# Kernel optimization log

Measured on AMD Instinct MI355X. Metric: run time of the kernel, lower is better.

## Reference

```python
import jax, jax.numpy as jnp
import numpy as np


def _greens(x, k0_raw, amp_raw):
    """Faithful TunableGreens: FFT-domain filtering with per-channel-pair Green's fn.
    NOTE: the source applies fftn over axes (0,1) (batch+H) but ifftn over axes (1,2)
    (H+W); we replicate that exactly."""
    H, W = x.shape[1], x.shape[2]
    k0 = jax.nn.softplus(k0_raw)    # (C, Co, 1, 1)
    amp = jax.nn.softplus(amp_raw)  # (C, Co, 1, 1)
    fy = (2.0 * jnp.pi) * jnp.fft.fftfreq(H, d=1.0).astype(jnp.float32)
    fx = (2.0 * jnp.pi) * jnp.fft.fftfreq(W, d=1.0).astype(jnp.float32)
    p = fy[:, None] ** 2 + fx[None, :] ** 2            # (H, W) = sum(freq_grid**2, -1)
    g_fourier = 1.0 / (amp * p - k0 - 1j)              # (C, Co, H, W) complex64
    u_fft = jnp.fft.fftn(x, axes=(0, 1))               # axes (0,1) as in source
    u_filtered = jnp.einsum('bijc,coij->bijo', u_fft, g_fourier)
    return jnp.fft.ifftn(u_filtered, axes=(1, 2)).real


def _D(Wm, x):
    # per-pixel channel mixing: x [b,i,j,c], Wm [b,i,j,c,o]
    return jnp.einsum('bijc,bijco->bijo', x, Wm)


def _project(k, W1, b1, W2, b2, W3, b3):
    act = lambda z: jnp.exp(-z ** 2)
    x = act(k @ W1 + b1)
    x = act(x @ W2 + b2)
    return x @ W3 + b3


def setup_inputs() -> dict:
    key = jax.random.key(0)
    ks = jax.random.split(key, 10)
    B, H, W, C = 2, 128, 128, 32
    d = {}
    d['u'] = jax.random.normal(ks[0], (B, H, W, C), jnp.float32)
    d['k'] = jax.random.normal(ks[1], (B, H, W, 1), jnp.float32)
    for i, n in enumerate(['g1', 'g2', 'g3', 'g4']):
        d[n] = jax.random.normal(ks[2 + i], (B, H, W, C, C), jnp.float32) * 0.1
    # Project MLP params (lecun-normal-ish scaling)
    d['W1'] = jax.random.normal(ks[6], (1, C), jnp.float32)
    d['b1'] = jnp.zeros((C,), jnp.float32)
    d['W2'] = jax.random.normal(ks[7], (C, C), jnp.float32) * (1.0 / np.sqrt(C))
    d['b2'] = jnp.zeros((C,), jnp.float32)
    d['W3'] = jax.random.normal(ks[8], (C, C), jnp.float32) * (1.0 / np.sqrt(C))
    d['b3'] = jnp.zeros((C,), jnp.float32)
    # TunableGreens params, constant(1.0) init as in source
    d['k0_G'] = jnp.ones((C, C, 1, 1), jnp.float32)
    d['amp_G'] = jnp.ones((C, C, 1, 1), jnp.float32)
    d['k0_Gs'] = jnp.ones((C, C, 1, 1), jnp.float32)
    d['amp_Gs'] = jnp.ones((C, C, 1, 1), jnp.float32)
    return d


def reference(u, k, g1, g2, g3, g4, W1, b1, W2, b2, W3, b3,
              k0_G, amp_G, k0_Gs, amp_Gs):
    s = _project(k, W1, b1, W2, b2, W3, b3)           # [B,H,W,C]
    u1 = _D(g4, _greens(s, k0_Gs, amp_Gs))
    u2 = _D(g1, _greens(_D(g2, u), k0_G, amp_G)) + _D(g3, u)
    return u1 + u2
```

## Files before the change

kernel.cpp:

```cpp
#include <hip/hip_runtime.h>

using u16 = unsigned short;
using u32 = unsigned int;

#define PI2 6.283185307179586f

struct cpx { float x, y; };

__device__ __forceinline__ float bf2f(u16 h){ return __uint_as_float(((u32)h) << 16); }
__device__ __forceinline__ u16 f2bf(float f){
  u32 u = __float_as_uint(f);
  u = u + 0x7fffu + ((u >> 16) & 1u);
  return (u16)(u >> 16);
}

__device__ __forceinline__ float ldv(const void* base, size_t i, int md){
  return md ? ((const float*)base)[i] : bf2f(((const u16*)base)[i]);
}

__device__ __forceinline__ cpx cadd(cpx a, cpx b){ return {a.x+b.x, a.y+b.y}; }
__device__ __forceinline__ cpx csub(cpx a, cpx b){ return {a.x-b.x, a.y-b.y}; }
__device__ __forceinline__ cpx cmul(cpx a, cpx b){ return {a.x*b.x - a.y*b.y, a.x*b.y + a.y*b.x}; }
__device__ __forceinline__ int br6(int l){ return (int)(__brev((u32)l) >> 26); }
__device__ __forceinline__ cpx shflx(cpx v, int m){
  cpx r; r.x = __shfl_xor(v.x, m, 64); r.y = __shfl_xor(v.y, m, 64); return r;
}

__device__ __forceinline__ void make_tw(int l, cpx tw[6]){
  #pragma unroll
  for (int s = 0; s < 6; s++){
    int h = 64 >> s;
    float ang = -PI2 * (float)(l & (h-1)) / (float)(2*h);
    float sv, cv; sincosf(ang, &sv, &cv);
    tw[s] = {cv, sv};
  }
}

__device__ __forceinline__ void fft_fwd(cpx& v0, cpx& v1, int l, const cpx tw[6]){
  cpx a = cadd(v0, v1), b = csub(v0, v1);
  v0 = a; v1 = cmul(b, tw[0]);
  #pragma unroll
  for (int s = 1; s < 6; s++){
    int h = 64 >> s;
    cpx p0 = shflx(v0, h), p1 = shflx(v1, h);
    bool up = (l & h) != 0;
    cpx n0 = up ? cmul(csub(p0, v0), tw[s]) : cadd(v0, p0);
    cpx n1 = up ? cmul(csub(p1, v1), tw[s]) : cadd(v1, p1);
    v0 = n0; v1 = n1;
  }
  { cpx p0 = shflx(v0, 1), p1 = shflx(v1, 1);
    bool up = (l & 1) != 0;
    v0 = up ? csub(p0, v0) : cadd(v0, p0);
    v1 = up ? csub(p1, v1) : cadd(v1, p1); }
}

__device__ __forceinline__ void fft_inv(cpx& v0, cpx& v1, int l, const cpx tw[6]){
  { cpx p0 = shflx(v0, 1), p1 = shflx(v1, 1);
    bool up = (l & 1) != 0;
    v0 = up ? csub(p0, v0) : cadd(v0, p0);
    v1 = up ? csub(p1, v1) : cadd(v1, p1); }
  #pragma unroll
  for (int s = 5; s >= 1; s--){
    int h = 64 >> s;
    cpx twc = {tw[s].x, -tw[s].y};
    cpx p0 = shflx(v0, h), p1 = shflx(v1, h);
    bool up = (l & h) != 0;
    cpx t0 = cmul(up ? v0 : p0, twc);
    cpx t1 = cmul(up ? v1 : p1, twc);
    v0 = up ? csub(p0, t0) : cadd(v0, t0);
    v1 = up ? csub(p1, t1) : cadd(v1, t1);
  }
  { cpx twc = {tw[0].x, -tw[0].y};
    cpx t = cmul(v1, twc);
    cpx n0 = cadd(v0, t), n1 = csub(v0, t);
    v0 = n0; v1 = n1; }
}

__device__ __forceinline__ float softplusf(float x){ return (x > 20.0f) ? x : log1pf(expf(x)); }

__device__ __forceinline__ void acc8_bf(uint4 a, uint4 b, float x0, float x1, float acc[8]){
  acc[0] = fmaf(x0, __uint_as_float(a.x << 16),         acc[0]);
  acc[1] = fmaf(x0, __uint_as_float(a.x & 0xffff0000u), acc[1]);
  acc[2] = fmaf(x0, __uint_as_float(a.y << 16),         acc[2]);
  acc[3] = fmaf(x0, __uint_as_float(a.y & 0xffff0000u), acc[3]);
  acc[4] = fmaf(x0, __uint_as_float(a.z << 16),         acc[4]);
  acc[5] = fmaf(x0, __uint_as_float(a.z & 0xffff0000u), acc[5]);
  acc[6] = fmaf(x0, __uint_as_float(a.w << 16),         acc[6]);
  acc[7] = fmaf(x0, __uint_as_float(a.w & 0xffff0000u), acc[7]);
  acc[0] = fmaf(x1, __uint_as_float(b.x << 16),         acc[0]);
  acc[1] = fmaf(x1, __uint_as_float(b.x & 0xffff0000u), acc[1]);
  acc[2] = fmaf(x1, __uint_as_float(b.y << 16),         acc[2]);
  acc[3] = fmaf(x1, __uint_as_float(b.y & 0xffff0000u), acc[3]);
  acc[4] = fmaf(x1, __uint_as_float(b.z << 16),         acc[4]);
  acc[5] = fmaf(x1, __uint_as_float(b.z & 0xffff0000u), acc[5]);
  acc[6] = fmaf(x1, __uint_as_float(b.w << 16),         acc[6]);
  acc[7] = fmaf(x1, __uint_as_float(b.w & 0xffff0000u), acc[7]);
}
__device__ __forceinline__ void acc8_f32(float4 a0, float4 a1, float4 b0, float4 b1,
                                         float x0, float x1, float acc[8]){
  acc[0] = fmaf(x0, a0.x, acc[0]); acc[1] = fmaf(x0, a0.y, acc[1]);
  acc[2] = fmaf(x0, a0.z, acc[2]); acc[3] = fmaf(x0, a0.w, acc[3]);
  acc[4] = fmaf(x0, a1.x, acc[4]); acc[5] = fmaf(x0, a1.y, acc[5]);
  acc[6] = fmaf(x0, a1.z, acc[6]); acc[7] = fmaf(x0, a1.w, acc[7]);
  acc[0] = fmaf(x1, b0.x, acc[0]); acc[1] = fmaf(x1, b0.y, acc[1]);
  acc[2] = fmaf(x1, b0.z, acc[2]); acc[3] = fmaf(x1, b0.w, acc[3]);
  acc[4] = fmaf(x1, b1.x, acc[4]); acc[5] = fmaf(x1, b1.y, acc[5]);
  acc[6] = fmaf(x1, b1.z, acc[6]); acc[7] = fmaf(x1, b1.w, acc[7]);
}

__global__ void k_detect(const void* g1, int* flag){
  __shared__ int cnt;
  if (threadIdx.x == 0) cnt = 0;
  __syncthreads();
  const u16* p = (const u16*)g1;
  int local = 0;
  for (int i = threadIdx.x; i < 4096; i += 256){
    float v = bf2f(p[i]);
    if (!(fabsf(v) < 100.0f)) local++;
  }
  atomicAdd(&cnt, local);
  __syncthreads();
  if (threadIdx.x == 0) *flag = (cnt > 64) ? 1 : 0;
}

__global__ void k_tabs(const void* k0G, const void* ampG, const void* k0Gs, const void* ampGs,
                       float* tabs, const int* flag){
  int md = *flag;
  for (int i = threadIdx.x; i < 1024; i += 256){
    tabs[i]        = softplusf(ldv(ampGs, i, md));
    tabs[1024 + i] = softplusf(ldv(k0Gs, i, md));
    tabs[2048 + i] = softplusf(ldv(ampG, i, md));
    tabs[3072 + i] = softplusf(ldv(k0G, i, md));
  }
}

__global__ __launch_bounds__(256) void k_project(const void* kin, const void* W1, const void* b1,
    const void* W2, const void* b2, const void* W3, const void* b3, float* S, const int* flag){
  __shared__ float sW2[1024], sW3[1024], sml[128];
  int md = *flag;
  int t = threadIdx.x;
  for (int i = t; i < 1024; i += 256){ sW2[i] = ldv(W2, i, md); sW3[i] = ldv(W3, i, md); }
  if (t < 32){
    sml[t]     = ldv(W1, t, md); sml[32+t] = ldv(b1, t, md);
    sml[64+t]  = ldv(b2, t, md); sml[96+t] = ldv(b3, t, md);
  }
  __syncthreads();
  int pix = blockIdx.x * 256 + t;
  float kv = ldv(kin, pix, md);
  float a1[32], a2[32];
  #pragma unroll
  for (int c = 0; c < 32; c++){ float z = fmaf(kv, sml[c], sml[32+c]); a1[c] = expf(-z*z); }
  for (int o = 0; o < 32; o++){
    float z = sml[64+o];
    #pragma unroll
    for (int c = 0; c < 32; c++) z = fmaf(a1[c], sW2[c*32+o], z);
    a2[o] = expf(-z*z);
  }
  for (int o = 0; o < 32; o++){
    float sv = sml[96+o];
    #pragma unroll
    for (int c = 0; c < 32; c++) sv = fmaf(a2[c], sW3[c*32+o], sv);
    S[(size_t)pix*32 + o] = sv;
  }
}

__global__ __launch_bounds__(256) void k_dmat(const void* u, const void* g2, float* D, const int* flag){
  int md = *flag;
  int t = threadIdx.x, l = t & 63;
  size_t pix = (size_t)blockIdx.x * 8 + (size_t)(t >> 6) * 2;
  int c32 = l & 31, ch = l >> 2;
  float xa = ldv(u, pix*32 + c32, md);
  float xb = ldv(u, (pix+1)*32 + c32, md);
  float acc0[8] = {0.f,0.f,0.f,0.f,0.f,0.f,0.f,0.f};
  float acc1[8] = {0.f,0.f,0.f,0.f,0.f,0.f,0.f,0.f};
  if (md){
    const float4* Ra = (const float4*)((const float*)g2 + pix*1024);
    const float4* Rb = (const float4*)((const float*)g2 + (pix+1)*1024);
    float4 aa = Ra[2*l], ab = Ra[2*l+1], ac = Ra[128+2*l], ad = Ra[128+2*l+1];
    float4 ba = Rb[2*l], bb = Rb[2*l+1], bc = Rb[128+2*l], bd = Rb[128+2*l+1];
    float xa0 = __shfl(xa, ch, 64), xa1 = __shfl(xa, 16+ch, 64);
    float xb0 = __shfl(xb, ch, 64), xb1 = __shfl(xb, 16+ch, 64);
    acc8_f32(aa, ab, ac, ad, xa0, xa1, acc0);
    acc8_f32(ba, bb, bc, bd, xb0, xb1, acc1);
  } else {
    const uint4* Ra = (const uint4*)((const u16*)g2 + pix*1024);
    const uint4* Rb = (const uint4*)((const u16*)g2 + (pix+1)*1024);
    uint4 a0 = Ra[l], a1 = Ra[64+l];
    uint4 b0 = Rb[l], b1 = Rb[64+l];
    float xa0 = __shfl(xa, ch, 64), xa1 = __shfl(xa, 16+ch, 64);
    float xb0 = __shfl(xb, ch, 64), xb1 = __shfl(xb, 16+ch, 64);
    acc8_bf(a0, a1, xa0, xa1, acc0);
    acc8_bf(b0, b1, xb0, xb1, acc1);
  }
  #pragma unroll
  for (int d = 4; d <= 32; d <<= 1){
    #pragma unroll
    for (int jj = 0; jj < 8; jj++){
      acc0[jj] += __shfl_xor(acc0[jj], d, 64);
      acc1[jj] += __shfl_xor(acc1[jj], d, 64);
    }
  }
  if (l < 4){
    ((float4*)(D + pix*32))[2*l]       = make_float4(acc0[0], acc0[1], acc0[2], acc0[3]);
    ((float4*)(D + pix*32))[2*l+1]     = make_float4(acc0[4], acc0[5], acc0[6], acc0[7]);
    ((float4*)(D + (pix+1)*32))[2*l]   = make_float4(acc1[0], acc1[1], acc1[2], acc1[3]);
    ((float4*)(D + (pix+1)*32))[2*l+1] = make_float4(acc1[4], acc1[5], acc1[6], acc1[7]);
  }
}

__global__ __launch_bounds__(512) void kg_a(const float* S, const float* Dd, const float* tabs, float2* Q){
  __shared__ __align__(16) cpx E[64*128];
  int t = threadIdx.x;
  int p = blockIdx.x >> 7, j = blockIdx.x & 127;
  const float* X = p ? Dd : S;
  const float* ampT = tabs + p*2048;
  const float* k0T  = ampT + 1024;
  int l = t & 63, w = t >> 6;
  cpx tw[6]; make_tw(l, tw);

  {
    int h = t >> 2, ch = (t & 3) * 8;
    const float4* x0 = (const float4*)(X + (((size_t)h)*128 + j)*32 + ch);
    const float4* x1 = (const float4*)(X + (((size_t)(128 + h))*128 + j)*32 + ch);
    #pragma unroll
    for (int q = 0; q < 2; q++){
      float4 A = x0[q], B = x1[q];
      int c = ch + q*4;
      E[(c+0)*128 + h] = {A.x+B.x, 0.f};  E[(32+c+0)*128 + h] = {A.x-B.x, 0.f};
      E[(c+1)*128 + h] = {A.y+B.y, 0.f};  E[(32+c+1)*128 + h] = {A.y-B.y, 0.f};
      E[(c+2)*128 + h] = {A.z+B.z, 0.f};  E[(32+c+2)*128 + h] = {A.z-B.z, 0.f};
      E[(c+3)*128 + h] = {A.w+B.w, 0.f};  E[(32+c+3)*128 + h] = {A.w-B.w, 0.f};
    }
  }
  __syncthreads();
  for (int c = w; c < 64; c += 8){
    cpx* col = E + c*128;
    cpx v0 = col[l], v1 = col[l+64];
    fft_fwd(v0, v1, l, tw);
    ((float4*)col)[br6(l)] = make_float4(v0.x, v0.y, v1.x, v1.y);
  }
  __syncthreads();
  {
    int o = t & 31, ig = t >> 5;
    float aT[32], kT[32];
    #pragma unroll
    for (int c = 0; c < 32; c++){ aT[c] = ampT[c*32+o]; kT[c] = k0T[c*32+o]; }
    float fj = (j < 64) ? (float)j : (float)(j - 128);
    fj *= (PI2 / 128.0f);
    float px = fj * fj;
    for (int chunk = 0; chunk < 2; chunk++){
      cpx y0[4], y1[4];
      #pragma unroll
      for (int q = 0; q < 4; q++){
        int i = ig + 16*(chunk*4 + q);
        float fi = (i < 64) ? (float)i : (float)(i - 128);
        fi *= (PI2 / 128.0f);
        float pp = fmaf(fi, fi, px);
        cpx a0 = {0.f, 0.f}, a1 = {0.f, 0.f};
        #pragma unroll
        for (int c = 0; c < 32; c++){
          float dd  = fmaf(aT[c], pp, -kT[c]);
          float inv = __builtin_amdgcn_rcpf(fmaf(dd, dd, 1.0f));
          float gr = dd * inv, gi = inv;
          cpx x0 = E[c*128 + i];
          cpx x1 = E[(32+c)*128 + i];
          a0.x = fmaf(x0.x, gr, fmaf(-x0.y, gi, a0.x));
          a0.y = fmaf(x0.x, gi, fmaf( x0.y, gr, a0.y));
          a1.x = fmaf(x1.x, gr, fmaf(-x1.y, gi, a1.x));
          a1.y = fmaf(x1.x, gi, fmaf( x1.y, gr, a1.y));
        }
        y0[q] = a0; y1[q] = a1;
      }
      __syncthreads();
      #pragma unroll
      for (int q = 0; q < 4; q++){
        int i = ig + 16*(chunk*4 + q);
        E[o*128 + i]      = y0[q];
        E[(32+o)*128 + i] = y1[q];
      }
      __syncthreads();
    }
  }
  for (int cidx = w; cidx < 64; cidx += 8){
    cpx* col = E + cidx*128;
    float4 tv = ((const float4*)col)[br6(l)];
    cpx v0 = {tv.x, tv.y}, v1 = {tv.z, tv.w};
    fft_inv(v0, v1, l, tw);
    const float sc = 1.0f/128.0f;
    col[l]    = {v0.x*sc, v0.y*sc};
    col[l+64] = {v1.x*sc, v1.y*sc};
  }
  __syncthreads();
  {
    int o = t & 31, bb = (t >> 5) & 1, yb = t >> 6;
    for (int m = 0; m < 16; m++){
      int y = yb + 8*m;
      cpx v = E[(bb*32+o)*128 + y];
      Q[((((size_t)(p*2+bb))*128 + y)*128 + j)*32 + o] = make_float2(v.x, v.y);
    }
  }
}

__global__ __launch_bounds__(256) void kg_c(const float2* Q, float* G0, float* G1){
  __shared__ __align__(16) cpx Z[32*128];
  __shared__ float R[32*128];
  int t = threadIdx.x, l = t & 63, w = t >> 6;
  int idx = blockIdx.x;
  int p = idx >> 8, rem = idx & 255, bb = rem >> 7, y = rem & 127;
  cpx tw[6]; make_tw(l, tw);
  const float4* src = (const float4*)(Q + ((size_t)((p*2+bb)*128 + y))*4096);
  for (int q = t; q < 2048; q += 256){
    float4 v = src[q];
    int m = q*2, jj = m >> 5, c = m & 31;
    Z[c*128 + jj]     = {v.x, v.y};
    Z[(c+1)*128 + jj] = {v.z, v.w};
  }
  __syncthreads();
  for (int c = w; c < 32; c += 4){
    cpx* col = Z + c*128;
    float4 tv = ((const float4*)col)[br6(l)];
    cpx v0 = {tv.x, tv.y}, v1 = {tv.z, tv.w};
    fft_inv(v0, v1, l, tw);
    R[c*128 + l]      = v0.x * (1.0f/128.0f);
    R[c*128 + l + 64] = v1.x * (1.0f/128.0f);
  }
  __syncthreads();
  float* dst = (p ? G1 : G0) + ((size_t)(bb*128 + y))*4096;
  int jj = t >> 3, c4 = (t & 7)*4;
  for (int rep = 0; rep < 4; rep++){
    int j2 = jj + rep*32;
    float4 o4 = { R[(c4+0)*128 + j2], R[(c4+1)*128 + j2],
                  R[(c4+2)*128 + j2], R[(c4+3)*128 + j2] };
    ((float4*)(dst + (size_t)j2*32))[c4 >> 2] = o4;
  }
}

__global__ __launch_bounds__(256) void k_final(const void* u, const void* g1, const void* g3, const void* g4,
    const float* G0, const float* G1, void* out, const int* flag){
  int md = *flag;
  int t = threadIdx.x, l = t & 63;
  size_t pix = (size_t)blockIdx.x * 4 + (t >> 6);
  int c32 = l & 31, ch = l >> 2;
  float xs = G0[pix*32 + c32];
  float xm = G1[pix*32 + c32];
  float xu = ldv(u, pix*32 + c32, md);
  float acc[8] = {0.f,0.f,0.f,0.f,0.f,0.f,0.f,0.f};
  if (md){
    const float4* R4 = (const float4*)((const float*)g4 + pix*1024);
    const float4* R1 = (const float4*)((const float*)g1 + pix*1024);
    const float4* R3 = (const float4*)((const float*)g3 + pix*1024);
    float4 p4a = R4[2*l], p4b = R4[2*l+1], q4a = R4[128+2*l], q4b = R4[128+2*l+1];
    float4 p1a = R1[2*l], p1b = R1[2*l+1], q1a = R1[128+2*l], q1b = R1[128+2*l+1];
    float4 p3a = R3[2*l], p3b = R3[2*l+1], q3a = R3[128+2*l], q3b = R3[128+2*l+1];
    float xs0 = __shfl(xs, ch, 64), xs1 = __shfl(xs, 16+ch, 64);
    float xm0 = __shfl(xm, ch, 64), xm1 = __shfl(xm, 16+ch, 64);
    float xu0 = __shfl(xu, ch, 64), xu1 = __shfl(xu, 16+ch, 64);
    acc8_f32(p4a, p4b, q4a, q4b, xs0, xs1, acc);
    acc8_f32(p1a, p1b, q1a, q1b, xm0, xm1, acc);
    acc8_f32(p3a, p3b, q3a, q3b, xu0, xu1, acc);
  } else {
    const uint4* R4 = (const uint4*)((const u16*)g4 + pix*1024);
    const uint4* R1 = (const uint4*)((const u16*)g1 + pix*1024);
    const uint4* R3 = (const uint4*)((const u16*)g3 + pix*1024);
    uint4 a4 = R4[l], b4 = R4[64+l];
    uint4 a1 = R1[l], b1 = R1[64+l];
    uint4 a3 = R3[l], b3 = R3[64+l];
    float xs0 = __shfl(xs, ch, 64), xs1 = __shfl(xs, 16+ch, 64);
    float xm0 = __shfl(xm, ch, 64), xm1 = __shfl(xm, 16+ch, 64);
    float xu0 = __shfl(xu, ch, 64), xu1 = __shfl(xu, 16+ch, 64);
    acc8_bf(a4, b4, xs0, xs1, acc);
    acc8_bf(a1, b1, xm0, xm1, acc);
    acc8_bf(a3, b3, xu0, xu1, acc);
  }
  #pragma unroll
  for (int d = 4; d <= 32; d <<= 1){
    #pragma unroll
    for (int jj = 0; jj < 8; jj++) acc[jj] += __shfl_xor(acc[jj], d, 64);
  }
  if (l < 4){
    if (md){
      float4 o0 = {acc[0], acc[1], acc[2], acc[3]};
      float4 o1 = {acc[4], acc[5], acc[6], acc[7]};
      ((float4*)out)[pix*8 + 2*l]     = o0;
      ((float4*)out)[pix*8 + 2*l + 1] = o1;
    } else {
      uint4 v;
      v.x = (u32)f2bf(acc[0]) | ((u32)f2bf(acc[1]) << 16);
      v.y = (u32)f2bf(acc[2]) | ((u32)f2bf(acc[3]) << 16);
      v.z = (u32)f2bf(acc[4]) | ((u32)f2bf(acc[5]) << 16);
      v.w = (u32)f2bf(acc[6]) | ((u32)f2bf(acc[7]) << 16);
      ((uint4*)out)[pix*4 + l] = v;
    }
  }
}

extern "C" void kernel_launch(void* const* d_in, const int* in_sizes, int n_in,
                              void* d_out, int out_size, void* d_ws, size_t ws_size,
                              hipStream_t stream){
  (void)in_sizes; (void)n_in; (void)out_size; (void)ws_size;
  const void* u    = d_in[0];
  const void* kk   = d_in[1];
  const void* g1   = d_in[2];
  const void* g2   = d_in[3];
  const void* g3   = d_in[4];
  const void* g4   = d_in[5];
  const void* W1   = d_in[6];
  const void* b1   = d_in[7];
  const void* W2   = d_in[8];
  const void* b2   = d_in[9];
  const void* W3   = d_in[10];
  const void* b3   = d_in[11];
  const void* k0G  = d_in[12];
  const void* ampG = d_in[13];
  const void* k0Gs = d_in[14];
  const void* ampGs= d_in[15];

  float* ws   = (float*)d_ws;
  float* S    = ws;
  float* Dd   = ws + (1u<<20);
  float2* Q   = (float2*)(ws + 2*(1u<<20));
  float* G0   = ws + 6*(1u<<20);
  float* G1b  = ws + 7*(1u<<20);
  float* tabs = ws + 8*(1u<<20);
  int*   flag = (int*)(tabs + 4096);

  k_detect <<<1,    256, 0, stream>>>(g1, flag);
  k_tabs   <<<1,    256, 0, stream>>>(k0G, ampG, k0Gs, ampGs, tabs, flag);
  k_project<<<128,  256, 0, stream>>>(kk, W1, b1, W2, b2, W3, b3, S, flag);
  k_dmat   <<<4096, 256, 0, stream>>>(u, g2, Dd, flag);
  kg_a     <<<256,  512, 0, stream>>>(S, Dd, tabs, Q);
  kg_c     <<<512,  256, 0, stream>>>(Q, G0, G1b);
  k_final  <<<8192, 256, 0, stream>>>(u, g1, g3, g4, G0, G1b, (void*)d_out, flag);
}
```

Measured before the change: 536.7 us.

## Software-pipeline per-pixel mixing kernels over multiple pixels per wave and pad FFT LDS

k_dmat and k_final now have each wave process several consecutive pixels (8 and 4), prefetching the next pixel's weight rows and inputs into registers while computing the current one, with grid sizes reduced to match. This targets memory latency in the bandwidth-bound channel-mixing kernels. kg_c pads its shared-memory column strides to cut LDS bank conflicts in the transpose and output gather. The prefetching raises register pressure, which may lower occupancy.

After: 541.5 us. About the same (+0.9%).

```diff
diff --git a/kernel.cpp b/kernel.cpp
--- a/kernel.cpp
+++ b/kernel.cpp
@@ -167,44 +167,85 @@
 __global__ __launch_bounds__(256) void k_dmat(const void* u, const void* g2, float* D, const int* flag){
   int md = *flag;
   int t = threadIdx.x, l = t & 63;
-  size_t pix = (size_t)blockIdx.x * 8 + (size_t)(t >> 6) * 2;
+  int wid = blockIdx.x * 4 + (t >> 6);
+  size_t base = (size_t)wid * 8;
   int c32 = l & 31, ch = l >> 2;
-  float xa = ldv(u, pix*32 + c32, md);
-  float xb = ldv(u, (pix+1)*32 + c32, md);
-  float acc0[8] = {0.f,0.f,0.f,0.f,0.f,0.f,0.f,0.f};
-  float acc1[8] = {0.f,0.f,0.f,0.f,0.f,0.f,0.f,0.f};
-  if (md){
-    const float4* Ra = (const float4*)((const float*)g2 + pix*1024);
-    const float4* Rb = (const float4*)((const float*)g2 + (pix+1)*1024);
-    float4 aa = Ra[2*l], ab = Ra[2*l+1], ac = Ra[128+2*l], ad = Ra[128+2*l+1];
-    float4 ba = Rb[2*l], bb = Rb[2*l+1], bc = Rb[128+2*l], bd = Rb[128+2*l+1];
-    float xa0 = __shfl(xa, ch, 64), xa1 = __shfl(xa, 16+ch, 64);
-    float xb0 = __shfl(xb, ch, 64), xb1 = __shfl(xb, 16+ch, 64);
-    acc8_f32(aa, ab, ac, ad, xa0, xa1, acc0);
-    acc8_f32(ba, bb, bc, bd, xb0, xb1, acc1);
+  const u16* U16 = (const u16*)u;
+  const float* U32 = (const float*)u;
+  if (!md){
+    const uint4* R = (const uint4*)((const u16*)g2 + base*1024);
+    uint4 a0 = R[l], a1 = R[64+l], b0 = R[128+l], b1 = R[192+l];
+    float xa = bf2f(U16[base*32 + c32]);
+    float xb = bf2f(U16[(base+1)*32 + c32]);
+    #pragma unroll
+    for (int it = 0; it < 4; it++){
+      int nit = (it < 3) ? it + 1 : it;
+      uint4 na0 = R[nit*256 + l],       na1 = R[nit*256 + 64 + l];
+      uint4 nb0 = R[nit*256 + 128 + l], nb1 = R[nit*256 + 192 + l];
+      float nxa = bf2f(U16[(base + 2*nit)*32 + c32]);
+      float nxb = bf2f(U16[(base + 2*nit + 1)*32 + c32]);
+      float xa0 = __shfl(xa, ch, 64), xa1 = __shfl(xa, 16+ch, 64);
+      float xb0 = __shfl(xb, ch, 64), xb1 = __shfl(xb, 16+ch, 64);
+      float acc0[8] = {0.f,0.f,0.f,0.f,0.f,0.f,0.f,0.f};
+      float acc1[8] = {0.f,0.f,0.f,0.f,0.f,0.f,0.f,0.f};
+      acc8_bf(a0, a1, xa0, xa1, acc0);
+      acc8_bf(b0, b1, xb0, xb1, acc1);
+      #pragma unroll
+      for (int d = 4; d <= 32; d <<= 1){
+        #pragma unroll
+        for (int jj = 0; jj < 8; jj++){
+          acc0[jj] += __shfl_xor(acc0[jj], d, 64);
+          acc1[jj] += __shfl_xor(acc1[jj], d, 64);
+        }
+      }
+      size_t p0 = base + 2*it, p1 = p0 + 1;
+      if (l < 4){
+        ((float4*)(D + p0*32))[2*l]   = make_float4(acc0[0], acc0[1], acc0[2], acc0[3]);
+        ((float4*)(D + p0*32))[2*l+1] = make_float4(acc0[4], acc0[5], acc0[6], acc0[7]);
+        ((float4*)(D + p1*32))[2*l]   = make_float4(acc1[0], acc1[1], acc1[2], acc1[3]);
+        ((float4*)(D + p1*32))[2*l+1] = make_float4(acc1[4], acc1[5], acc1[6], acc1[7]);
+      }
+      a0 = na0; a1 = na1; b0 = nb0; b1 = nb1; xa = nxa; xb = nxb;
+    }
   } else {
-    const uint4* Ra = (const uint4*)((const u16*)g2 + pix*1024);
-    const uint4* Rb = (const uint4*)((const u16*)g2 + (pix+1)*1024);
-    uint4 a0 = Ra[l], a1 = Ra[64+l];
-    uint4 b0 = Rb[l], b1 = Rb[64+l];
-    float xa0 = __shfl(xa, ch, 64), xa1 = __shfl(xa, 16+ch, 64);
-    float xb0 = __shfl(xb, ch, 64), xb1 = __shfl(xb, 16+ch, 64);
-    acc8_bf(a0, a1, xa0, xa1, acc0);
-    acc8_bf(b0, b1, xb0, xb1, acc1);
-  }
-  #pragma unroll
-  for (int d = 4; d <= 32; d <<= 1){
-    #pragma unroll
-    for (int jj = 0; jj < 8; jj++){
-      acc0[jj] += __shfl_xor(acc0[jj], d, 64);
-      acc1[jj] += __shfl_xor(acc1[jj], d, 64);
-    }
-  }
-  if (l < 4){
-    ((float4*)(D + pix*32))[2*l]       = make_float4(acc0[0], acc0[1], acc0[2], acc0[3]);
-    ((float4*)(D + pix*32))[2*l+1]     = make_float4(acc0[4], acc0[5], acc0[6], acc0[7]);
-    ((float4*)(D + (pix+1)*32))[2*l]   = make_float4(acc1[0], acc1[1], acc1[2], acc1[3]);
-    ((float4*)(D + (pix+1)*32))[2*l+1] = make_float4(acc1[4], acc1[5], acc1[6], acc1[7]);
+    const float4* R = (const float4*)((const float*)g2 + base*1024);
+    float4 a0 = R[2*l], a1 = R[2*l+1], a2 = R[128+2*l], a3 = R[128+2*l+1];
+    float4 b0 = R[256+2*l], b1 = R[256+2*l+1], b2 = R[384+2*l], b3 = R[384+2*l+1];
+    float xa = U32[base*32 + c32];
+    float xb = U32[(base+1)*32 + c32];
+    #pragma unroll
+    for (int it = 0; it < 4; it++){
+      int nit = (it < 3) ? it + 1 : it;
+      const float4* Rn = R + nit*512;
+      float4 na0 = Rn[2*l], na1 = Rn[2*l+1], na2 = Rn[128+2*l], na3 = Rn[128+2*l+1];
+      float4 nb0 = Rn[256+2*l], nb1 = Rn[256+2*l+1], nb2 = Rn[384+2*l], nb3 = Rn[384+2*l+1];
+      float nxa = U32[(base + 2*nit)*32 + c32];
+      float nxb = U32[(base + 2*nit + 1)*32 + c32];
+      float xa0 = __shfl(xa, ch, 64), xa1 = __shfl(xa, 16+ch, 64);
+      float xb0 = __shfl(xb, ch, 64), xb1 = __shfl(xb, 16+ch, 64);
+      float acc0[8] = {0.f,0.f,0.f,0.f,0.f,0.f,0.f,0.f};
+      float acc1[8] = {0.f,0.f,0.f,0.f,0.f,0.f,0.f,0.f};
+      acc8_f32(a0, a1, a2, a3, xa0, xa1, acc0);
+      acc8_f32(b0, b1, b2, b3, xb0, xb1, acc1);
+      #pragma unroll
+      for (int d = 4; d <= 32; d <<= 1){
+        #pragma unroll
+        for (int jj = 0; jj < 8; jj++){
+          acc0[jj] += __shfl_xor(acc0[jj], d, 64);
+          acc1[jj] += __shfl_xor(acc1[jj], d, 64);
+        }
+      }
+      size_t p0 = base + 2*it, p1 = p0 + 1;
+      if (l < 4){
+        ((float4*)(D + p0*32))[2*l]   = make_float4(acc0[0], acc0[1], acc0[2], acc0[3]);
+        ((float4*)(D + p0*32))[2*l+1] = make_float4(acc0[4], acc0[5], acc0[6], acc0[7]);
+        ((float4*)(D + p1*32))[2*l]   = make_float4(acc1[0], acc1[1], acc1[2], acc1[3]);
+        ((float4*)(D + p1*32))[2*l+1] = make_float4(acc1[4], acc1[5], acc1[6], acc1[7]);
+      }
+      a0 = na0; a1 = na1; a2 = na2; a3 = na3;
+      b0 = nb0; b1 = nb1; b2 = nb2; b3 = nb3;
+      xa = nxa; xb = nxb;
+    }
   }
 }
 
@@ -301,9 +342,11 @@
   }
 }
 
+#define ZS 130
+#define RS 133
 __global__ __launch_bounds__(256) void kg_c(const float2* Q, float* G0, float* G1){
-  __shared__ __align__(16) cpx Z[32*128];
-  __shared__ float R[32*128];
+  __shared__ __align__(16) cpx Z[32*ZS];
+  __shared__ float R[32*RS];
   int t = threadIdx.x, l = t & 63, w = t >> 6;
   int idx = blockIdx.x;
   int p = idx >> 8, rem = idx & 255, bb = rem >> 7, y = rem & 127;
@@ -312,25 +355,25 @@
   for (int q = t; q < 2048; q += 256){
     float4 v = src[q];
     int m = q*2, jj = m >> 5, c = m & 31;
-    Z[c*128 + jj]     = {v.x, v.y};
-    Z[(c+1)*128 + jj] = {v.z, v.w};
+    Z[c*ZS + jj]     = {v.x, v.y};
+    Z[(c+1)*ZS + jj] = {v.z, v.w};
   }
   __syncthreads();
   for (int c = w; c < 32; c += 4){
-    cpx* col = Z + c*128;
+    cpx* col = Z + c*ZS;
     float4 tv = ((const float4*)col)[br6(l)];
     cpx v0 = {tv.x, tv.y}, v1 = {tv.z, tv.w};
     fft_inv(v0, v1, l, tw);
-    R[c*128 + l]      = v0.x * (1.0f/128.0f);
-    R[c*128 + l + 64] = v1.x * (1.0f/128.0f);
+    R[c*RS + l]      = v0.x * (1.0f/128.0f);
+    R[c*RS + l + 64] = v1.x * (1.0f/128.0f);
   }
   __syncthreads();
   float* dst = (p ? G1 : G0) + ((size_t)(bb*128 + y))*4096;
   int jj = t >> 3, c4 = (t & 7)*4;
   for (int rep = 0; rep < 4; rep++){
     int j2 = jj + rep*32;
-    float4 o4 = { R[(c4+0)*128 + j2], R[(c4+1)*128 + j2],
-                  R[(c4+2)*128 + j2], R[(c4+3)*128 + j2] };
+    float4 o4 = { R[(c4+0)*RS + j2], R[(c4+1)*RS + j2],
+                  R[(c4+2)*RS + j2], R[(c4+3)*RS + j2] };
     ((float4*)(dst + (size_t)j2*32))[c4 >> 2] = o4;
   }
 }
@@ -339,57 +382,95 @@
     const float* G0, const float* G1, void* out, const int* flag){
   int md = *flag;
   int t = threadIdx.x, l = t & 63;
-  size_t pix = (size_t)blockIdx.x * 4 + (t >> 6);
+  int wid = blockIdx.x * 4 + (t >> 6);
+  size_t base = (size_t)wid * 4;
   int c32 = l & 31, ch = l >> 2;
-  float xs = G0[pix*32 + c32];
-  float xm = G1[pix*32 + c32];
-  float xu = ldv(u, pix*32 + c32, md);
-  float acc[8] = {0.f,0.f,0.f,0.f,0.f,0.f,0.f,0.f};
-  if (md){
-    const float4* R4 = (const float4*)((const float*)g4 + pix*1024);
-    const float4* R1 = (const float4*)((const float*)g1 + pix*1024);
-    const float4* R3 = (const float4*)((const float*)g3 + pix*1024);
+  if (!md){
+    const u16* U = (const u16*)u;
+    const uint4* R4 = (const uint4*)((const u16*)g4 + base*1024);
+    const uint4* R1 = (const uint4*)((const u16*)g1 + base*1024);
+    const uint4* R3 = (const uint4*)((const u16*)g3 + base*1024);
+    uint4 a4 = R4[l], b4 = R4[64+l];
+    uint4 a1 = R1[l], b1 = R1[64+l];
+    uint4 a3 = R3[l], b3 = R3[64+l];
+    float xs = G0[base*32 + c32], xm = G1[base*32 + c32], xu = bf2f(U[base*32 + c32]);
+    #pragma unroll
+    for (int it = 0; it < 4; it++){
+      int nit = (it < 3) ? it + 1 : it;
+      uint4 na4 = R4[nit*128 + l], nb4 = R4[nit*128 + 64 + l];
+      uint4 na1 = R1[nit*128 + l], nb1 = R1[nit*128 + 64 + l];
+      uint4 na3 = R3[nit*128 + l], nb3 = R3[nit*128 + 64 + l];
+      float nxs = G0[(base+nit)*32 + c32];
+      float nxm = G1[(base+nit)*32 + c32];
+      float nxu = bf2f(U[(base+nit)*32 + c32]);
+      float xs0 = __shfl(xs, ch, 64), xs1 = __shfl(xs, 16+ch, 64);
+      float xm0 = __shfl(xm, ch, 64), xm1 = __shfl(xm, 16+ch, 64);
+      float xu0 = __shfl(xu, ch, 64), xu1 = __shfl(xu, 16+ch, 64);
+      float acc[8] = {0.f,0.f,0.f,0.f,0.f,0.f,0.f,0.f};
+      acc8_bf(a4, b4, xs0, xs1, acc);
+      acc8_bf(a1, b1, xm0, xm1, acc);
+      acc8_bf(a3, b3, xu0, xu1, acc);
+      #pragma unroll
+      for (int d = 4; d <= 32; d <<= 1){
+        #pragma unroll
+        for (int jj = 0; jj < 8; jj++) acc[jj] += __shfl_xor(acc[jj], d, 64);
+      }
+      size_t pix = base + it;
+      if (l < 4){
+        uint4 v;
+        v.x = (u32)f2bf(acc[0]) | ((u32)f2bf(acc[1]) << 16);
+        v.y = (u32)f2bf(acc[2]) | ((u32)f2bf(acc[3]) << 16);
+        v.z = (u32)f2bf(acc[4]) | ((u32)f2bf(acc[5]) << 16);
+        v.w = (u32)f2bf(acc[6]) | ((u32)f2bf(acc[7]) << 16);
+        ((uint4*)out)[pix*4 + l] = v;
+      }
+      a4 = na4; b4 = nb4; a1 = na1; b1 = nb1; a3 = na3; b3 = nb3;
+      xs = nxs; xm = nxm; xu = nxu;
+    }
+  } else {
+    const float* U = (const float*)u;
+    const float4* R4 = (const float4*)((const float*)g4 + base*1024);
+    const float4* R1 = (const float4*)((const float*)g1 + base*1024);
+    const float4* R3 = (const float4*)((const float*)g3 + base*1024);
     float4 p4a = R4[2*l], p4b = R4[2*l+1], q4a = R4[128+2*l], q4b = R4[128+2*l+1];
     float4 p1a = R1[2*l], p1b = R1[2*l+1], q1a = R1[128+2*l], q1b = R1[128+2*l+1];
     float4 p3a = R3[2*l], p3b = R3[2*l+1], q3a = R3[128+2*l], q3b = R3[128+2*l+1];
-    float xs0 = __shfl(xs, ch, 64), xs1 = __shfl(xs, 16+ch, 64);
-    float xm0 = __shfl(xm, ch, 64), xm1 = __shfl(xm, 16+ch, 64);
-    float xu0 = __shfl(xu, ch, 64), xu1 = __shfl(xu, 16+ch, 64);
-    acc8_f32(p4a, p4b, q4a, q4b, xs0, xs1, acc);
-    acc8_f32(p1a, p1b, q1a, q1b, xm0, xm1, acc);
-    acc8_f32(p3a, p3b, q3a, q3b, xu0, xu1, acc);
-  } else {
-    const uint4* R4 = (const uint4*)((const u16*)g4 + pix*1024);
-    const uint4* R1 = (const uint4*)((const u16*)g1 + pix*1024);
-    const uint4* R3 = (const uint4*)((const u16*)g3 + pix*1024);
-    uint4 a4 = R4[l], b4 = R4[64+l];
-    uint4 a1 = R1[l], b1 = R1[64+l];
-    uint4 a3 = R3[l], b3 = R3[64+l];
-    float xs0 = __shfl(xs, ch, 64), xs1 = __shfl(xs, 16+ch, 64);
-    float xm0 = __shfl(xm, ch, 64), xm1 = __shfl(xm, 16+ch, 64);
-    float xu0 = __shfl(xu, ch, 64), xu1 = __shfl(xu, 16+ch, 64);
-    acc8_bf(a4, b4, xs0, xs1, acc);
-    acc8_bf(a1, b1, xm0, xm1, acc);
-    acc8_bf(a3, b3, xu0, xu1, acc);
-  }
-  #pragma unroll
-  for (int d = 4; d <= 32; d <<= 1){
-    #pragma unroll
-    for (int jj = 0; jj < 8; jj++) acc[jj] += __shfl_xor(acc[jj], d, 64);
-  }
-  if (l < 4){
-    if (md){
-      float4 o0 = {acc[0], acc[1], acc[2], acc[3]};
-      float4 o1 = {acc[4], acc[5], acc[6], acc[7]};
-      ((float4*)out)[pix*8 + 2*l]     = o0;
-      ((float4*)out)[pix*8 + 2*l + 1] = o1;
-    } else {
-      uint4 v;
-      v.x = (u32)f2bf(acc[0]) | ((u32)f2bf(acc[1]) << 16);
-      v.y = (u32)f2bf(acc[2]) | ((u32)f2bf(acc[3]) << 16);
-      v.z = (u32)f2bf(acc[4]) | ((u32)f2bf(acc[5]) << 16);
-      v.w = (u32)f2bf(acc[6]) | ((u32)f2bf(acc[7]) << 16);
-      ((uint4*)out)[pix*4 + l] = v;
+    float xs = G0[base*32 + c32], xm = G1[base*32 + c32], xu = U[base*32 + c32];
+    #pragma unroll
+    for (int it = 0; it < 4; it++){
+      int nit = (it < 3) ? it + 1 : it;
+      const float4* R4n = R4 + nit*256;
+      const float4* R1n = R1 + nit*256;
+      const float4* R3n = R3 + nit*256;
+      float4 n4a = R4n[2*l], n4b = R4n[2*l+1], m4a = R4n[128+2*l], m4b = R4n[128+2*l+1];
+      float4 n1a = R1n[2*l], n1b = R1n[2*l+1], m1a = R1n[128+2*l], m1b = R1n[128+2*l+1];
+      float4 n3a = R3n[2*l], n3b = R3n[2*l+1], m3a = R3n[128+2*l], m3b = R3n[128+2*l+1];
+      float nxs = G0[(base+nit)*32 + c32];
+      float nxm = G1[(base+nit)*32 + c32];
+      float nxu = U[(base+nit)*32 + c32];
+      float xs0 = __shfl(xs, ch, 64), xs1 = __shfl(xs, 16+ch, 64);
+      float xm0 = __shfl(xm, ch, 64), xm1 = __shfl(xm, 16+ch, 64);
+      float xu0 = __shfl(xu, ch, 64), xu1 = __shfl(xu, 16+ch, 64);
+      float acc[8] = {0.f,0.f,0.f,0.f,0.f,0.f,0.f,0.f};
+      acc8_f32(p4a, p4b, q4a, q4b, xs0, xs1, acc);
+      acc8_f32(p1a, p1b, q1a, q1b, xm0, xm1, acc);
+      acc8_f32(p3a, p3b, q3a, q3b, xu0, xu1, acc);
+      #pragma unroll
+      for (int d = 4; d <= 32; d <<= 1){
+        #pragma unroll
+        for (int jj = 0; jj < 8; jj++) acc[jj] += __shfl_xor(acc[jj], d, 64);
+      }
+      size_t pix = base + it;
+      if (l < 4){
+        float4 o0 = {acc[0], acc[1], acc[2], acc[3]};
+        float4 o1 = {acc[4], acc[5], acc[6], acc[7]};
+        ((float4*)out)[pix*8 + 2*l]     = o0;
+        ((float4*)out)[pix*8 + 2*l + 1] = o1;
+      }
+      p4a = n4a; p4b = n4b; q4a = m4a; q4b = m4b;
+      p1a = n1a; p1b = n1b; q1a = m1a; q1b = m1b;
+      p3a = n3a; p3b = n3b; q3a = m3a; q3b = m3b;
+      xs = nxs; xm = nxm; xu = nxu;
     }
   }
 }
@@ -427,8 +508,8 @@
   k_detect <<<1,    256, 0, stream>>>(g1, flag);
   k_tabs   <<<1,    256, 0, stream>>>(k0G, ampG, k0Gs, ampGs, tabs, flag);
   k_project<<<128,  256, 0, stream>>>(kk, W1, b1, W2, b2, W3, b3, S, flag);
-  k_dmat   <<<4096, 256, 0, stream>>>(u, g2, Dd, flag);
+  k_dmat   <<<1024, 256, 0, stream>>>(u, g2, Dd, flag);
   kg_a     <<<256,  512, 0, stream>>>(S, Dd, tabs, Q);
   kg_c     <<<512,  256, 0, stream>>>(Q, G0, G1b);
-  k_final  <<<8192, 256, 0, stream>>>(u, g1, g3, g4, G0, G1b, (void*)d_out, flag);
-}
+  k_final  <<<2048, 256, 0, stream>>>(u, g1, g3, g4, G0, G1b, (void*)d_out, flag);
+}
```
